# Performance work log

Measured on AMD Instinct MI355X. Metric: run time of the kernel, lower is better.

Reference implementation:

```python
import jax, jax.numpy as jnp
import numpy as np

EPS = 1e-5
NEG_SLOPE = 0.2  # GATConv default negative_slope


def layer_norm(x, g, b):
    mu = jnp.mean(x, axis=-1, keepdims=True)
    var = jnp.mean((x - mu) ** 2, axis=-1, keepdims=True)
    return (x - mu) * jax.lax.rsqrt(var + EPS) * g + b


def setup_inputs() -> dict:
    key = jax.random.key(0)
    ks = jax.random.split(key, 16)
    B, NPG = 64, 1024          # graphs, fine nodes per graph
    NF = B * NPG               # 65536 fine nodes
    IN, HID, ATT, H, LLM = 1024, 1024, 64, 8, 2048
    D = ATT * H                # 512
    w = lambda k, shp: (jax.random.normal(k, shp, jnp.float32) * 0.02)
    # structured bipartite star edges: fine node i -> global node i // NPG
    edge_index = jnp.stack([jnp.arange(NF, dtype=jnp.int32),
                            (jnp.arange(NF, dtype=jnp.int32) // NPG)])
    return {
        "x_fine": jax.random.normal(ks[0], (NF, IN), jnp.float32),
        "x_global": jax.random.normal(ks[1], (B, D), jnp.float32),
        "edge_index_fine_global": edge_index,
        "nf_g": jnp.ones((IN,), jnp.float32), "nf_b": jnp.zeros((IN,), jnp.float32),
        "ip_w1": w(ks[2], (IN, HID)), "ip_b1": jnp.zeros((HID,), jnp.float32),
        "ip_w2": w(ks[3], (HID, D)), "ip_b2": jnp.zeros((D,), jnp.float32),
        "ng_g": jnp.ones((D,), jnp.float32), "ng_b": jnp.zeros((D,), jnp.float32),
        "gat_ws": w(ks[4], (D, D)), "gat_wd": w(ks[5], (D, D)),
        "att_s": w(ks[6], (1, H, ATT)), "att_d": w(ks[7], (1, H, ATT)),
        "gat_bias": jnp.zeros((D,), jnp.float32),
        "gp_w": w(ks[8], (D, LLM)), "gp_b": jnp.zeros((LLM,), jnp.float32),
        "fp_w": w(ks[9], (D, LLM)), "fp_b": jnp.zeros((LLM,), jnp.float32),
    }


def reference(x_fine, x_global, edge_index_fine_global,
              nf_g, nf_b, ip_w1, ip_b1, ip_w2, ip_b2, ng_g, ng_b,
              gat_ws, gat_wd, att_s, att_d, gat_bias,
              gp_w, gp_b, fp_w, fp_b):
    B = x_global.shape[0]
    H = att_s.shape[1]
    C = x_global.shape[1] // H

    # fine branch: LayerNorm -> MLP projection to H*C
    xf = layer_norm(x_fine, nf_g, nf_b)
    xf = jax.nn.relu(xf @ ip_w1 + ip_b1) @ ip_w2 + ip_b2      # [NF, H*C]
    xg = layer_norm(x_global, ng_g, ng_b)                      # [B, H*C]

    # bipartite GATConv (eval mode: attention dropout disabled)
    xs = (xf @ gat_ws).reshape(-1, H, C)                       # [NF, H, C]
    xd = (xg @ gat_wd).reshape(B, H, C)                        # [B, H, C]
    a_s = jnp.sum(xs * att_s, axis=-1)                         # [NF, H]
    a_d = jnp.sum(xd * att_d, axis=-1)                         # [B, H]

    row, col = edge_index_fine_global[0], edge_index_fine_global[1]
    loops = jnp.arange(B, dtype=row.dtype)                     # add_self_loops: nodes < min(NF,B)
    rows = jnp.concatenate([row, loops])
    cols = jnp.concatenate([col, loops])
    # PyG removes pre-existing self-loop edges; emulate by masking them out
    self_mask = jnp.concatenate([row == col, jnp.zeros((B,), bool)])

    logits = jax.nn.leaky_relu(a_s[rows] + a_d[cols], NEG_SLOPE)   # [E+B, H]
    logits = jnp.where(self_mask[:, None], -jnp.inf, logits)
    m = jax.ops.segment_max(logits, cols, num_segments=B)         # [B, H]
    e = jnp.exp(logits - m[cols])
    e = jnp.where(self_mask[:, None], 0.0, e)
    denom = jax.ops.segment_sum(e, cols, num_segments=B)
    alpha = e / denom[cols]                                       # [E+B, H]

    msg = xs[rows] * alpha[..., None]                              # [E+B, H, C]
    agg = jax.ops.segment_sum(msg, cols, num_segments=B)          # [B, H, C]
    xg = agg.reshape(B, H * C) + gat_bias + xg                    # GAT out + residual

    og = (xg @ gp_w + gp_b)[:, None, :]                            # [B, 1, LLM]
    of = (xf @ fp_w + fp_b).reshape(B, -1, fp_w.shape[1])          # [B, NPG, LLM]
    return jnp.concatenate([og, of], axis=1)                       # [B, 1+NPG, LLM]
```

## Files before the change

### kernel.cpp

```cpp
#include <hip/hip_runtime.h>
#include <hip/hip_bf16.h>
#include <math.h>

typedef __bf16 bf16_t;
typedef bf16_t bf16x8 __attribute__((ext_vector_type(8)));
typedef bf16_t bf16x4 __attribute__((ext_vector_type(4)));
typedef float f32x4 __attribute__((ext_vector_type(4)));

#define DEVINL __device__ __forceinline__

DEVINL float wave_reduce_sum(float v) {
#pragma unroll
  for (int o = 32; o > 0; o >>= 1) v += __shfl_down(v, o);
  return v;
}
DEVINL float wave_reduce_max(float v) {
#pragma unroll
  for (int o = 32; o > 0; o >>= 1) v = fmaxf(v, __shfl_down(v, o));
  return v;
}
DEVINL float block_reduce_sum256(float v, float* red) {
  int tid = threadIdx.x;
  __syncthreads();
  v = wave_reduce_sum(v);
  if ((tid & 63) == 0) red[tid >> 6] = v;
  __syncthreads();
  return red[0] + red[1] + red[2] + red[3];
}
DEVINL float block_reduce_max256(float v, float* red) {
  int tid = threadIdx.x;
  __syncthreads();
  v = wave_reduce_max(v);
  if ((tid & 63) == 0) red[tid >> 6] = v;
  __syncthreads();
  return fmaxf(fmaxf(red[0], red[1]), fmaxf(red[2], red[3]));
}

template <int CPT, bool BF16OUT>
__global__ __launch_bounds__(256) void k_ln(const float* __restrict__ x,
                                            const float* __restrict__ g,
                                            const float* __restrict__ b,
                                            void* __restrict__ out) {
  constexpr int COLS = CPT * 256;
  __shared__ float red[8];
  const size_t row = blockIdx.x;
  const float* xr = x + row * COLS;
  const int c0 = threadIdx.x * CPT;
  float v[CPT];
#pragma unroll
  for (int j = 0; j < CPT; j++) v[j] = xr[c0 + j];
  float s = 0;
#pragma unroll
  for (int j = 0; j < CPT; j++) s += v[j];
  const float mu = block_reduce_sum256(s, red) * (1.0f / COLS);
  float q = 0;
#pragma unroll
  for (int j = 0; j < CPT; j++) { float d = v[j] - mu; q += d * d; }
  const float var = block_reduce_sum256(q, red) * (1.0f / COLS);
  const float rs = rsqrtf(var + 1e-5f);
  if constexpr (BF16OUT) {
    bf16x4 o;
#pragma unroll
    for (int j = 0; j < CPT; j++)
      o[j] = (bf16_t)((v[j] - mu) * rs * g[c0 + j] + b[c0 + j]);
    *(bf16x4*)((bf16_t*)out + row * COLS + c0) = o;
  } else {
#pragma unroll
    for (int j = 0; j < CPT; j++)
      ((float*)out)[row * COLS + c0 + j] = (v[j] - mu) * rs * g[c0 + j] + b[c0 + j];
  }
}

__global__ __launch_bounds__(256) void k_tcast(const float* __restrict__ src,
                                               bf16_t* __restrict__ dst, int K, int N) {
  __shared__ float t[32][33];
  const int n0 = blockIdx.x * 32, k0 = blockIdx.y * 32;
  const int tx = threadIdx.x, ty = threadIdx.y;
#pragma unroll
  for (int i = 0; i < 32; i += 8)
    t[ty + i][tx] = src[(size_t)(k0 + ty + i) * N + n0 + tx];
  __syncthreads();
#pragma unroll
  for (int i = 0; i < 32; i += 8)
    dst[(size_t)(n0 + ty + i) * K + k0 + tx] = (bf16_t)t[tx][ty + i];
}

__global__ __launch_bounds__(256) void k_fold_wd(const float* __restrict__ gat_wd,
                                                 const float* __restrict__ att_d,
                                                 float* __restrict__ wd_att) {
  const int k = blockIdx.x * 256 + threadIdx.x;
#pragma unroll
  for (int h = 0; h < 8; h++) {
    float s = 0;
    for (int c = 0; c < 64; c++)
      s += gat_wd[(size_t)k * 512 + h * 64 + c] * att_d[h * 64 + c];
    wd_att[k * 8 + h] = s;
  }
}

template <int N, int K, int EPI>
__global__ __launch_bounds__(256, 2) void gemm_bt(const bf16_t* __restrict__ A,
                                                  const bf16_t* __restrict__ Bt,
                                                  const float* __restrict__ bias,
                                                  void* __restrict__ Cout) {
  __shared__ bf16_t As[128 * 64];
  __shared__ bf16_t Bs[128 * 64];
  const int tid = threadIdx.x;
  const int lane = tid & 63;
  const int wid = tid >> 6;
  const int wm = wid >> 1, wn = wid & 1;
  const size_t arow0 = (size_t)blockIdx.x * 128;
  const int bcol0 = blockIdx.y * 128;

  f32x4 acc[4][4] = {};
  const int kTiles = K / 64;
  for (int kt = 0; kt < kTiles; ++kt) {
    const int k0 = kt * 64;
#pragma unroll
    for (int i = 0; i < 4; ++i) {
      const int c = i * 256 + tid;
      const int r = c >> 3, kc = (c & 7) * 8;
      const bf16_t* ga = A + (arow0 + r) * K + k0 + kc;
      __builtin_amdgcn_global_load_lds(
          (const __attribute__((address_space(1))) void*)ga,
          (__attribute__((address_space(3))) void*)(As + c * 8), 16, 0, 0);
      const bf16_t* gb = Bt + ((size_t)bcol0 + r) * K + k0 + kc;
      __builtin_amdgcn_global_load_lds(
          (const __attribute__((address_space(1))) void*)gb,
          (__attribute__((address_space(3))) void*)(Bs + c * 8), 16, 0, 0);
    }
    __syncthreads();
#pragma unroll
    for (int kk = 0; kk < 2; ++kk) {
      bf16x8 af[4], bfr[4];
      const int kofs = kk * 32 + (lane >> 4) * 8;
#pragma unroll
      for (int m = 0; m < 4; ++m)
        af[m] = *(const bf16x8*)(As + (wm * 64 + m * 16 + (lane & 15)) * 64 + kofs);
#pragma unroll
      for (int n = 0; n < 4; ++n)
        bfr[n] = *(const bf16x8*)(Bs + (wn * 64 + n * 16 + (lane & 15)) * 64 + kofs);
#pragma unroll
      for (int m = 0; m < 4; ++m)
#pragma unroll
        for (int n = 0; n < 4; ++n)
          acc[m][n] = __builtin_amdgcn_mfma_f32_16x16x32_bf16(af[m], bfr[n], acc[m][n], 0, 0, 0);
    }
    __syncthreads();
  }
  const int lr = (lane >> 4) * 4;
  const int lc = lane & 15;
#pragma unroll
  for (int n = 0; n < 4; ++n) {
    const int col = bcol0 + wn * 64 + n * 16 + lc;
    const float bv = (EPI == 2) ? 0.0f : bias[col];
#pragma unroll
    for (int m = 0; m < 4; ++m) {
#pragma unroll
      for (int j = 0; j < 4; ++j) {
        const size_t row = arow0 + wm * 64 + m * 16 + lr + j;
        float v = acc[m][n][j] + bv;
        if constexpr (EPI == 0) v = v > 0.0f ? v : 0.0f;
        if constexpr (EPI == 3) {
          const size_t orow = row + (row >> 10) + 1;
          ((float*)Cout)[orow * (size_t)N + col] = v;
        } else {
          ((bf16_t*)Cout)[row * (size_t)N + col] = (bf16_t)v;
        }
      }
    }
  }
}

__global__ __launch_bounds__(256) void k_attn(const bf16_t* __restrict__ xs,
                                              const float* __restrict__ xg,
                                              const float* __restrict__ wd_att,
                                              const float* __restrict__ att_s,
                                              float* __restrict__ agg) {
  const int b = blockIdx.x >> 3, h = blockIdx.x & 7;
  const int tid = threadIdx.x;
  __shared__ float sl[1024];
  __shared__ float part[256];
  __shared__ float red[8];
  __shared__ float s_att[64];
  __shared__ float s_sc[4];
  if (tid < 64) s_att[tid] = att_s[h * 64 + tid];
  float pa = 0;
#pragma unroll
  for (int kk = 0; kk < 2; kk++) {
    const int k = tid + kk * 256;
    pa += xg[b * 512 + k] * wd_att[k * 8 + h];
  }
  const float a_d = block_reduce_sum256(pa, red);
  const bf16_t* xsb = xs + ((size_t)b * 1024) * 512 + h * 64;
#pragma unroll
  for (int j = 0; j < 4; j++) {
    const int i = tid + j * 256;
    const bf16_t* xr = xsb + (size_t)i * 512;
    float s = 0;
#pragma unroll
    for (int c = 0; c < 64; c += 8) {
      bf16x8 v = *(const bf16x8*)(xr + c);
#pragma unroll
      for (int u = 0; u < 8; u++) s += (float)v[u] * s_att[c + u];
    }
    const float lg = s + a_d;
    sl[i] = lg > 0.0f ? lg : 0.2f * lg;
  }
  if (tid == 0) {
    float self_lg = -INFINITY;
    if (b != 0) {
      const bf16_t* xr = xs + (size_t)b * 512 + h * 64;
      float s = 0;
      for (int c = 0; c < 64; c++) s += (float)xr[c] * s_att[c];
      const float lg = s + a_d;
      self_lg = lg > 0.0f ? lg : 0.2f * lg;
    }
    s_sc[0] = self_lg;
  }
  __syncthreads();
  float mx = -1e30f;
#pragma unroll
  for (int j = 0; j < 4; j++) mx = fmaxf(mx, sl[tid + j * 256]);
  mx = block_reduce_max256(mx, red);
  const float m = fmaxf(mx, s_sc[0]);
  float ps = 0;
#pragma unroll
  for (int j = 0; j < 4; j++) {
    const int i = tid + j * 256;
    const float e = __expf(sl[i] - m);
    sl[i] = e;
    ps += e;
  }
  if (tid == 0) s_sc[1] = __expf(s_sc[0] - m);
  const float dsum = block_reduce_sum256(ps, red);
  const float e_self = s_sc[1];
  const float inv = 1.0f / (dsum + e_self);
  const int c = tid & 63, grp = tid >> 6;
  float acc = 0;
  const bf16_t* xcol = xs + ((size_t)b * 1024) * 512 + h * 64 + c;
  for (int i = grp * 256; i < grp * 256 + 256; i++)
    acc += sl[i] * (float)xcol[(size_t)i * 512];
  if (grp == 0) acc += e_self * (float)xs[(size_t)b * 512 + h * 64 + c];
  part[tid] = acc;
  __syncthreads();
  if (tid < 64) {
    const float t = part[tid] + part[tid + 64] + part[tid + 128] + part[tid + 192];
    agg[(size_t)b * 512 + h * 64 + tid] = t * inv;
  }
}

__global__ __launch_bounds__(256) void k_og(const float* __restrict__ agg,
                                            const float* __restrict__ gat_bias,
                                            const float* __restrict__ xg,
                                            const float* __restrict__ gp_w,
                                            const float* __restrict__ gp_b,
                                            float* __restrict__ out) {
  __shared__ float xv[512];
  const int b = blockIdx.y;
  const int c = blockIdx.x * 256 + threadIdx.x;
  for (int k = threadIdx.x; k < 512; k += 256)
    xv[k] = agg[b * 512 + k] + gat_bias[k] + xg[b * 512 + k];
  __syncthreads();
  float acc = gp_b[c];
#pragma unroll 8
  for (int k = 0; k < 512; k++) acc += xv[k] * gp_w[(size_t)k * 2048 + c];
  out[(size_t)b * 1025 * 2048 + c] = acc;
}

extern "C" void kernel_launch(void* const* d_in, const int* in_sizes, int n_in,
                              void* d_out, int out_size, void* d_ws, size_t ws_size,
                              hipStream_t stream) {
  const float* x_fine   = (const float*)d_in[0];
  const float* x_global = (const float*)d_in[1];
  const float* nf_g  = (const float*)d_in[3];
  const float* nf_b  = (const float*)d_in[4];
  const float* ip_w1 = (const float*)d_in[5];
  const float* ip_b1 = (const float*)d_in[6];
  const float* ip_w2 = (const float*)d_in[7];
  const float* ip_b2 = (const float*)d_in[8];
  const float* ng_g  = (const float*)d_in[9];
  const float* ng_b  = (const float*)d_in[10];
  const float* gat_ws   = (const float*)d_in[11];
  const float* gat_wd   = (const float*)d_in[12];
  const float* att_s    = (const float*)d_in[13];
  const float* att_d    = (const float*)d_in[14];
  const float* gat_bias = (const float*)d_in[15];
  const float* gp_w = (const float*)d_in[16];
  const float* gp_b = (const float*)d_in[17];
  const float* fp_w = (const float*)d_in[18];
  const float* fp_b = (const float*)d_in[19];
  float* out = (float*)d_out;

  char* ws = (char*)d_ws;
  bf16_t* xf_ln = (bf16_t*)ws;
  bf16_t* hbuf  = (bf16_t*)(ws + 134217728ULL);
  char* sm = ws + 268435456ULL;
  bf16_t* w1t = (bf16_t*)sm;
  bf16_t* w2t = (bf16_t*)(sm + 2097152ULL);
  bf16_t* wst = (bf16_t*)(sm + 3145728ULL);
  bf16_t* fpt = (bf16_t*)(sm + 3670016ULL);
  float*  xg  = (float*)(sm + 5767168ULL);
  float*  wd_att = (float*)(sm + 5898240ULL);
  float*  aggp   = (float*)(sm + 5914624ULL);
  bf16_t* xf  = xf_ln;
  bf16_t* xsb = hbuf;

  k_tcast<<<dim3(32, 32), dim3(32, 8), 0, stream>>>(ip_w1, w1t, 1024, 1024);
  k_tcast<<<dim3(16, 32), dim3(32, 8), 0, stream>>>(ip_w2, w2t, 1024, 512);
  k_tcast<<<dim3(16, 16), dim3(32, 8), 0, stream>>>(gat_ws, wst, 512, 512);
  k_tcast<<<dim3(64, 16), dim3(32, 8), 0, stream>>>(fp_w, fpt, 512, 2048);
  k_fold_wd<<<2, 256, 0, stream>>>(gat_wd, att_d, wd_att);

  k_ln<4, true><<<65536, 256, 0, stream>>>(x_fine, nf_g, nf_b, xf_ln);
  k_ln<2, false><<<64, 256, 0, stream>>>(x_global, ng_g, ng_b, xg);

  gemm_bt<1024, 1024, 0><<<dim3(512, 8), 256, 0, stream>>>(xf_ln, w1t, ip_b1, hbuf);
  gemm_bt<512, 1024, 1><<<dim3(512, 4), 256, 0, stream>>>(hbuf, w2t, ip_b2, xf);
  gemm_bt<512, 512, 2><<<dim3(512, 4), 256, 0, stream>>>(xf, wst, nullptr, xsb);

  k_attn<<<512, 256, 0, stream>>>(xsb, xg, wd_att, att_s, aggp);
  k_og<<<dim3(8, 64), 256, 0, stream>>>(aggp, gat_bias, xg, gp_w, gp_b, out);

  gemm_bt<2048, 512, 3><<<dim3(512, 16), 256, 0, stream>>>(xf, fpt, fp_b, out);
}
```

Measured before the change: 849.1 us.

## Fold GAT source projection into attention and use persistent double-buffered GEMM

```diff
diff --git a/kernel.cpp b/kernel.cpp
--- a/kernel.cpp
+++ b/kernel.cpp
@@ -14,11 +14,6 @@
   for (int o = 32; o > 0; o >>= 1) v += __shfl_down(v, o);
   return v;
 }
-DEVINL float wave_reduce_max(float v) {
-#pragma unroll
-  for (int o = 32; o > 0; o >>= 1) v = fmaxf(v, __shfl_down(v, o));
-  return v;
-}
 DEVINL float block_reduce_sum256(float v, float* red) {
   int tid = threadIdx.x;
   __syncthreads();
@@ -26,14 +21,6 @@
   if ((tid & 63) == 0) red[tid >> 6] = v;
   __syncthreads();
   return red[0] + red[1] + red[2] + red[3];
-}
-DEVINL float block_reduce_max256(float v, float* red) {
-  int tid = threadIdx.x;
-  __syncthreads();
-  v = wave_reduce_max(v);
-  if ((tid & 63) == 0) red[tid >> 6] = v;
-  __syncthreads();
-  return fmaxf(fmaxf(red[0], red[1]), fmaxf(red[2], red[3]));
 }
 
 template <int CPT, bool BF16OUT>
@@ -85,182 +72,254 @@
     dst[(size_t)(n0 + ty + i) * K + k0 + tx] = (bf16_t)t[tx][ty + i];
 }
 
-__global__ __launch_bounds__(256) void k_fold_wd(const float* __restrict__ gat_wd,
-                                                 const float* __restrict__ att_d,
-                                                 float* __restrict__ wd_att) {
+__global__ __launch_bounds__(256) void k_fold(const float* __restrict__ W,
+                                              const float* __restrict__ att,
+                                              float* __restrict__ out) {
   const int k = blockIdx.x * 256 + threadIdx.x;
 #pragma unroll
   for (int h = 0; h < 8; h++) {
     float s = 0;
     for (int c = 0; c < 64; c++)
-      s += gat_wd[(size_t)k * 512 + h * 64 + c] * att_d[h * 64 + c];
-    wd_att[k * 8 + h] = s;
+      s += W[(size_t)k * 512 + h * 64 + c] * att[h * 64 + c];
+    out[k * 8 + h] = s;
   }
 }
 
 template <int N, int K, int EPI>
-__global__ __launch_bounds__(256, 2) void gemm_bt(const bf16_t* __restrict__ A,
+__global__ __launch_bounds__(256, 2) void gemm_pm(const bf16_t* __restrict__ A,
                                                   const bf16_t* __restrict__ Bt,
                                                   const float* __restrict__ bias,
                                                   void* __restrict__ Cout) {
-  __shared__ bf16_t As[128 * 64];
-  __shared__ bf16_t Bs[128 * 64];
-  const int tid = threadIdx.x;
-  const int lane = tid & 63;
-  const int wid = tid >> 6;
+  constexpr int NBY = N / 128;
+  constexpr int WPC = 512 / NBY;
+  constexpr int TPW = 512 / WPC;
+  constexpr int nt = K / 64;
+  constexpr int NSTEP = TPW * nt;
+  __shared__ __align__(16) bf16_t As[2][8192];
+  __shared__ __align__(16) bf16_t Bs[2][8192];
+  const int w = blockIdx.x;
+  const int by = w % NBY;
+  const int mchunk = w / NBY;
+  const int tid = threadIdx.x, lane = tid & 63, wid = tid >> 6;
   const int wm = wid >> 1, wn = wid & 1;
-  const size_t arow0 = (size_t)blockIdx.x * 128;
-  const int bcol0 = blockIdx.y * 128;
+  const int bcol0 = by * 128;
+  const size_t mbase = (size_t)mchunk * TPW * 128;
+
+  int s_r[4], s_c[4];
+#pragma unroll
+  for (int i = 0; i < 4; i++) {
+    const int q = i * 256 + tid;
+    s_r[i] = q >> 3;
+    s_c[i] = ((q & 7) ^ ((q >> 3) & 7)) * 8;
+  }
+  const int l15 = lane & 15, l7 = lane & 7, lq = lane >> 4;
+  const int e0 = (lq ^ l7) * 8;
+  const int e1 = ((4 + lq) ^ l7) * 8;
+
+  float bv[4];
+#pragma unroll
+  for (int n = 0; n < 4; n++)
+    bv[n] = (EPI == 2) ? 0.0f : bias[bcol0 + wn * 64 + n * 16 + l15];
 
   f32x4 acc[4][4] = {};
-  const int kTiles = K / 64;
-  for (int kt = 0; kt < kTiles; ++kt) {
-    const int k0 = kt * 64;
-#pragma unroll
-    for (int i = 0; i < 4; ++i) {
-      const int c = i * 256 + tid;
-      const int r = c >> 3, kc = (c & 7) * 8;
-      const bf16_t* ga = A + (arow0 + r) * K + k0 + kc;
-      __builtin_amdgcn_global_load_lds(
-          (const __attribute__((address_space(1))) void*)ga,
-          (__attribute__((address_space(3))) void*)(As + c * 8), 16, 0, 0);
-      const bf16_t* gb = Bt + ((size_t)bcol0 + r) * K + k0 + kc;
-      __builtin_amdgcn_global_load_lds(
-          (const __attribute__((address_space(1))) void*)gb,
-          (__attribute__((address_space(3))) void*)(Bs + c * 8), 16, 0, 0);
-    }
-    __syncthreads();
-#pragma unroll
-    for (int kk = 0; kk < 2; ++kk) {
-      bf16x8 af[4], bfr[4];
-      const int kofs = kk * 32 + (lane >> 4) * 8;
-#pragma unroll
-      for (int m = 0; m < 4; ++m)
-        af[m] = *(const bf16x8*)(As + (wm * 64 + m * 16 + (lane & 15)) * 64 + kofs);
-#pragma unroll
-      for (int n = 0; n < 4; ++n)
-        bfr[n] = *(const bf16x8*)(Bs + (wn * 64 + n * 16 + (lane & 15)) * 64 + kofs);
-#pragma unroll
-      for (int m = 0; m < 4; ++m)
-#pragma unroll
-        for (int n = 0; n < 4; ++n)
-          acc[m][n] = __builtin_amdgcn_mfma_f32_16x16x32_bf16(af[m], bfr[n], acc[m][n], 0, 0, 0);
-    }
-    __syncthreads();
-  }
-  const int lr = (lane >> 4) * 4;
-  const int lc = lane & 15;
-#pragma unroll
-  for (int n = 0; n < 4; ++n) {
-    const int col = bcol0 + wn * 64 + n * 16 + lc;
-    const float bv = (EPI == 2) ? 0.0f : bias[col];
-#pragma unroll
-    for (int m = 0; m < 4; ++m) {
-#pragma unroll
-      for (int j = 0; j < 4; ++j) {
-        const size_t row = arow0 + wm * 64 + m * 16 + lr + j;
-        float v = acc[m][n][j] + bv;
-        if constexpr (EPI == 0) v = v > 0.0f ? v : 0.0f;
-        if constexpr (EPI == 3) {
-          const size_t orow = row + (row >> 10) + 1;
-          ((float*)Cout)[orow * (size_t)N + col] = v;
-        } else {
-          ((bf16_t*)Cout)[row * (size_t)N + col] = (bf16_t)v;
+
+#define STG(s, bb)                                                                   \
+  {                                                                                  \
+    const int _t = (s) / nt, _kt = (s) % nt;                                         \
+    _Pragma("unroll") for (int _i = 0; _i < 4; _i++) {                               \
+      const bf16_t* _ga =                                                            \
+          A + (mbase + _t * 128 + s_r[_i]) * (size_t)K + _kt * 64 + s_c[_i];         \
+      __builtin_amdgcn_global_load_lds(                                              \
+          (const __attribute__((address_space(1))) void*)_ga,                        \
+          (__attribute__((address_space(3))) void*)&As[bb][(_i * 256 + tid) * 8],    \
+          16, 0, 0);                                                                 \
+      const bf16_t* _gb =                                                            \
+          Bt + ((size_t)bcol0 + s_r[_i]) * (size_t)K + _kt * 64 + s_c[_i];           \
+      __builtin_amdgcn_global_load_lds(                                              \
+          (const __attribute__((address_space(1))) void*)_gb,                        \
+          (__attribute__((address_space(3))) void*)&Bs[bb][(_i * 256 + tid) * 8],    \
+          16, 0, 0);                                                                 \
+    }                                                                                \
+  }
+
+  STG(0, 0);
+  for (int s = 0; s < NSTEP; ++s) {
+    if (s + 1 < NSTEP) {
+      STG(s + 1, (s + 1) & 1);
+      asm volatile("s_waitcnt vmcnt(8)" ::: "memory");
+    } else {
+      asm volatile("s_waitcnt vmcnt(0)" ::: "memory");
+    }
+    __builtin_amdgcn_s_barrier();
+    const int b = s & 1;
+    bf16x8 af0[4], af1[4], bf0[4], bf1[4];
+#pragma unroll
+    for (int m = 0; m < 4; m++) {
+      const bf16_t* p = &As[b][(wm * 64 + m * 16 + l15) * 64];
+      af0[m] = *(const bf16x8*)(p + e0);
+      af1[m] = *(const bf16x8*)(p + e1);
+    }
+#pragma unroll
+    for (int n = 0; n < 4; n++) {
+      const bf16_t* p = &Bs[b][(wn * 64 + n * 16 + l15) * 64];
+      bf0[n] = *(const bf16x8*)(p + e0);
+      bf1[n] = *(const bf16x8*)(p + e1);
+    }
+#pragma unroll
+    for (int m = 0; m < 4; m++)
+#pragma unroll
+      for (int n = 0; n < 4; n++) {
+        acc[m][n] = __builtin_amdgcn_mfma_f32_16x16x32_bf16(af0[m], bf0[n], acc[m][n], 0, 0, 0);
+        acc[m][n] = __builtin_amdgcn_mfma_f32_16x16x32_bf16(af1[m], bf1[n], acc[m][n], 0, 0, 0);
+      }
+    if ((s & (nt - 1)) == nt - 1) {
+      const int t = s / nt;
+      const int lr = lq * 4;
+#pragma unroll
+      for (int n = 0; n < 4; n++) {
+        const int col = bcol0 + wn * 64 + n * 16 + l15;
+#pragma unroll
+        for (int m = 0; m < 4; m++) {
+#pragma unroll
+          for (int j = 0; j < 4; j++) {
+            const size_t row = mbase + (size_t)t * 128 + wm * 64 + m * 16 + lr + j;
+            float v = acc[m][n][j] + bv[n];
+            if (EPI == 0) v = v > 0.0f ? v : 0.0f;
+            if (EPI == 3) {
+              const size_t orow = row + (row >> 10) + 1;
+              ((float*)Cout)[orow * (size_t)N + col] = v;
+            } else {
+              ((bf16_t*)Cout)[row * (size_t)N + col] = (bf16_t)v;
+            }
+            acc[m][n][j] = 0.0f;
+          }
         }
       }
     }
-  }
-}
-
-__global__ __launch_bounds__(256) void k_attn(const bf16_t* __restrict__ xs,
-                                              const float* __restrict__ xg,
-                                              const float* __restrict__ wd_att,
-                                              const float* __restrict__ att_s,
-                                              float* __restrict__ agg) {
-  const int b = blockIdx.x >> 3, h = blockIdx.x & 7;
-  const int tid = threadIdx.x;
-  __shared__ float sl[1024];
-  __shared__ float part[256];
-  __shared__ float red[8];
-  __shared__ float s_att[64];
-  __shared__ float s_sc[4];
-  if (tid < 64) s_att[tid] = att_s[h * 64 + tid];
+    __builtin_amdgcn_s_barrier();
+  }
+#undef STG
+}
+
+__global__ __launch_bounds__(256) void k_as(const bf16_t* __restrict__ xf,
+                                            const float* __restrict__ wsatt,
+                                            float* __restrict__ a_s) {
+  const int tid = threadIdx.x, l = tid & 63, wid = tid >> 6;
+  float wreg[64];
+#pragma unroll
+  for (int q = 0; q < 16; q++) {
+    const float4 v = *(const float4*)(wsatt + l * 64 + q * 4);
+    wreg[q * 4 + 0] = v.x; wreg[q * 4 + 1] = v.y;
+    wreg[q * 4 + 2] = v.z; wreg[q * 4 + 3] = v.w;
+  }
+  const size_t base = (size_t)blockIdx.x * 128 + wid * 32;
+  for (int rr = 0; rr < 32; rr++) {
+    const size_t i = base + rr;
+    const bf16x8 v = *(const bf16x8*)(xf + i * 512 + l * 8);
+    float p[8] = {};
+#pragma unroll
+    for (int u = 0; u < 8; u++) {
+      const float xv = (float)v[u];
+#pragma unroll
+      for (int h = 0; h < 8; h++) p[h] += xv * wreg[u * 8 + h];
+    }
+#pragma unroll
+    for (int h = 0; h < 8; h++)
+#pragma unroll
+      for (int mk = 1; mk < 64; mk <<= 1) p[h] += __shfl_xor(p[h], mk);
+    float outv = 0.0f;
+#pragma unroll
+    for (int h = 0; h < 8; h++) outv = (l == h) ? p[h] : outv;
+    if (l < 8) a_s[i * 8 + l] = outv;
+  }
+}
+
+__global__ __launch_bounds__(512) void k_alpha_z(const float* __restrict__ a_s,
+                                                 const bf16_t* __restrict__ xf,
+                                                 const float* __restrict__ xg,
+                                                 const float* __restrict__ wd_att,
+                                                 float* __restrict__ z) {
+  __shared__ float sal[8][1028];
+  const int b = blockIdx.x;
+  const int tid = threadIdx.x, l = tid & 63, h = tid >> 6;
   float pa = 0;
 #pragma unroll
-  for (int kk = 0; kk < 2; kk++) {
-    const int k = tid + kk * 256;
-    pa += xg[b * 512 + k] * wd_att[k * 8 + h];
-  }
-  const float a_d = block_reduce_sum256(pa, red);
-  const bf16_t* xsb = xs + ((size_t)b * 1024) * 512 + h * 64;
-#pragma unroll
-  for (int j = 0; j < 4; j++) {
-    const int i = tid + j * 256;
-    const bf16_t* xr = xsb + (size_t)i * 512;
-    float s = 0;
-#pragma unroll
-    for (int c = 0; c < 64; c += 8) {
-      bf16x8 v = *(const bf16x8*)(xr + c);
-#pragma unroll
-      for (int u = 0; u < 8; u++) s += (float)v[u] * s_att[c + u];
-    }
-    const float lg = s + a_d;
-    sl[i] = lg > 0.0f ? lg : 0.2f * lg;
-  }
-  if (tid == 0) {
-    float self_lg = -INFINITY;
-    if (b != 0) {
-      const bf16_t* xr = xs + (size_t)b * 512 + h * 64;
-      float s = 0;
-      for (int c = 0; c < 64; c++) s += (float)xr[c] * s_att[c];
-      const float lg = s + a_d;
-      self_lg = lg > 0.0f ? lg : 0.2f * lg;
-    }
-    s_sc[0] = self_lg;
-  }
-  __syncthreads();
-  float mx = -1e30f;
-#pragma unroll
-  for (int j = 0; j < 4; j++) mx = fmaxf(mx, sl[tid + j * 256]);
-  mx = block_reduce_max256(mx, red);
-  const float m = fmaxf(mx, s_sc[0]);
+  for (int u = 0; u < 8; u++)
+    pa += xg[b * 512 + l * 8 + u] * wd_att[(l * 8 + u) * 8 + h];
+#pragma unroll
+  for (int mk = 1; mk < 64; mk <<= 1) pa += __shfl_xor(pa, mk);
+  const float ad = pa;
+  const float* asb = a_s + (size_t)b * 1024 * 8;
+  float lg[16];
+  float lmax = -1e30f;
+#pragma unroll
+  for (int j = 0; j < 16; j++) {
+    const float a = asb[(l + j * 64) * 8 + h] + ad;
+    lg[j] = a > 0.0f ? a : 0.2f * a;
+    lmax = fmaxf(lmax, lg[j]);
+  }
+  float lself = -INFINITY;
+  if (l == 0 && b != 0) {
+    const float a = a_s[b * 8 + h] + ad;
+    lself = a > 0.0f ? a : 0.2f * a;
+  }
+  lmax = fmaxf(lmax, lself);
+#pragma unroll
+  for (int mk = 1; mk < 64; mk <<= 1) lmax = fmaxf(lmax, __shfl_xor(lmax, mk));
   float ps = 0;
 #pragma unroll
-  for (int j = 0; j < 4; j++) {
-    const int i = tid + j * 256;
-    const float e = __expf(sl[i] - m);
-    sl[i] = e;
-    ps += e;
-  }
-  if (tid == 0) s_sc[1] = __expf(s_sc[0] - m);
-  const float dsum = block_reduce_sum256(ps, red);
-  const float e_self = s_sc[1];
-  const float inv = 1.0f / (dsum + e_self);
-  const int c = tid & 63, grp = tid >> 6;
+  for (int j = 0; j < 16; j++) { lg[j] = __expf(lg[j] - lmax); ps += lg[j]; }
+  const float eself = (l == 0 && lself != -INFINITY) ? __expf(lself - lmax) : 0.0f;
+  ps += eself;
+#pragma unroll
+  for (int mk = 1; mk < 64; mk <<= 1) ps += __shfl_xor(ps, mk);
+  const float inv = 1.0f / ps;
+#pragma unroll
+  for (int j = 0; j < 16; j++) sal[h][l + j * 64] = lg[j] * inv;
+  if (l == 0) sal[h][1024] = eself * inv;
+  __syncthreads();
+  float zp[8] = {};
+  const bf16_t* xb = xf + (size_t)b * 1024 * 512 + l * 8;
+  for (int i = 0; i < 1024; i++) {
+    const float a = sal[h][i];
+    const bf16x8 v = *(const bf16x8*)(xb + (size_t)i * 512);
+#pragma unroll
+    for (int u = 0; u < 8; u++) zp[u] += a * (float)v[u];
+  }
+  {
+    const float a = sal[h][1024];
+    const bf16x8 v = *(const bf16x8*)(xf + (size_t)b * 512 + l * 8);
+#pragma unroll
+    for (int u = 0; u < 8; u++) zp[u] += a * (float)v[u];
+  }
+  float4 o0 = {zp[0], zp[1], zp[2], zp[3]};
+  float4 o1 = {zp[4], zp[5], zp[6], zp[7]};
+  float* zo = z + ((size_t)b * 8 + h) * 512 + l * 8;
+  *(float4*)zo = o0;
+  *(float4*)(zo + 4) = o1;
+}
+
+__global__ __launch_bounds__(512) void k_fin(const float* __restrict__ z,
+                                             const float* __restrict__ ws,
+                                             const float* __restrict__ gat_bias,
+                                             const float* __restrict__ xg,
+                                             float* __restrict__ aggx) {
+  const int b = blockIdx.x, c = threadIdx.x, h = c >> 6;
+  const float* zr = z + ((size_t)b * 8 + h) * 512;
   float acc = 0;
-  const bf16_t* xcol = xs + ((size_t)b * 1024) * 512 + h * 64 + c;
-  for (int i = grp * 256; i < grp * 256 + 256; i++)
-    acc += sl[i] * (float)xcol[(size_t)i * 512];
-  if (grp == 0) acc += e_self * (float)xs[(size_t)b * 512 + h * 64 + c];
-  part[tid] = acc;
-  __syncthreads();
-  if (tid < 64) {
-    const float t = part[tid] + part[tid + 64] + part[tid + 128] + part[tid + 192];
-    agg[(size_t)b * 512 + h * 64 + tid] = t * inv;
-  }
-}
-
-__global__ __launch_bounds__(256) void k_og(const float* __restrict__ agg,
-                                            const float* __restrict__ gat_bias,
-                                            const float* __restrict__ xg,
+#pragma unroll 8
+  for (int k = 0; k < 512; k++) acc += zr[k] * ws[(size_t)k * 512 + c];
+  aggx[b * 512 + c] = acc + gat_bias[c] + xg[b * 512 + c];
+}
+
+__global__ __launch_bounds__(256) void k_og(const float* __restrict__ aggx,
                                             const float* __restrict__ gp_w,
                                             const float* __restrict__ gp_b,
                                             float* __restrict__ out) {
   __shared__ float xv[512];
   const int b = blockIdx.y;
   const int c = blockIdx.x * 256 + threadIdx.x;
-  for (int k = threadIdx.x; k < 512; k += 256)
-    xv[k] = agg[b * 512 + k] + gat_bias[k] + xg[b * 512 + k];
+  for (int k = threadIdx.x; k < 512; k += 256) xv[k] = aggx[b * 512 + k];
   __syncthreads();
   float acc = gp_b[c];
 #pragma unroll 8
@@ -296,31 +355,33 @@
   bf16_t* xf_ln = (bf16_t*)ws;
   bf16_t* hbuf  = (bf16_t*)(ws + 134217728ULL);
   char* sm = ws + 268435456ULL;
-  bf16_t* w1t = (bf16_t*)sm;
-  bf16_t* w2t = (bf16_t*)(sm + 2097152ULL);
-  bf16_t* wst = (bf16_t*)(sm + 3145728ULL);
-  bf16_t* fpt = (bf16_t*)(sm + 3670016ULL);
-  float*  xg  = (float*)(sm + 5767168ULL);
-  float*  wd_att = (float*)(sm + 5898240ULL);
-  float*  aggp   = (float*)(sm + 5914624ULL);
-  bf16_t* xf  = xf_ln;
-  bf16_t* xsb = hbuf;
+  bf16_t* w1t  = (bf16_t*)sm;
+  bf16_t* w2t  = (bf16_t*)(sm + 2097152ULL);
+  bf16_t* fpt  = (bf16_t*)(sm + 3145728ULL);
+  float*  a_s  = (float*)(sm + 5242880ULL);
+  float*  xg   = (float*)(sm + 7340032ULL);
+  float*  wd_att = (float*)(sm + 7471104ULL);
+  float*  wsatt  = (float*)(sm + 7487488ULL);
+  float*  zbuf   = (float*)(sm + 7503872ULL);
+  float*  aggx   = (float*)(sm + 8552448ULL);
+  bf16_t* xf = xf_ln;
 
   k_tcast<<<dim3(32, 32), dim3(32, 8), 0, stream>>>(ip_w1, w1t, 1024, 1024);
   k_tcast<<<dim3(16, 32), dim3(32, 8), 0, stream>>>(ip_w2, w2t, 1024, 512);
-  k_tcast<<<dim3(16, 16), dim3(32, 8), 0, stream>>>(gat_ws, wst, 512, 512);
   k_tcast<<<dim3(64, 16), dim3(32, 8), 0, stream>>>(fp_w, fpt, 512, 2048);
-  k_fold_wd<<<2, 256, 0, stream>>>(gat_wd, att_d, wd_att);
+  k_fold<<<2, 256, 0, stream>>>(gat_wd, att_d, wd_att);
+  k_fold<<<2, 256, 0, stream>>>(gat_ws, att_s, wsatt);
 
   k_ln<4, true><<<65536, 256, 0, stream>>>(x_fine, nf_g, nf_b, xf_ln);
   k_ln<2, false><<<64, 256, 0, stream>>>(x_global, ng_g, ng_b, xg);
 
-  gemm_bt<1024, 1024, 0><<<dim3(512, 8), 256, 0, stream>>>(xf_ln, w1t, ip_b1, hbuf);
-  gemm_bt<512, 1024, 1><<<dim3(512, 4), 256, 0, stream>>>(hbuf, w2t, ip_b2, xf);
-  gemm_bt<512, 512, 2><<<dim3(512, 4), 256, 0, stream>>>(xf, wst, nullptr, xsb);
-
-  k_attn<<<512, 256, 0, stream>>>(xsb, xg, wd_att, att_s, aggp);
-  k_og<<<dim3(8, 64), 256, 0, stream>>>(aggp, gat_bias, xg, gp_w, gp_b, out);
-
-  gemm_bt<2048, 512, 3><<<dim3(512, 16), 256, 0, stream>>>(xf, fpt, fp_b, out);
-}
+  gemm_pm<1024, 1024, 0><<<512, 256, 0, stream>>>(xf_ln, w1t, ip_b1, hbuf);
+  gemm_pm<512, 1024, 1><<<512, 256, 0, stream>>>(hbuf, w2t, ip_b2, xf);
+
+  k_as<<<512, 256, 0, stream>>>(xf, wsatt, a_s);
+  k_alpha_z<<<64, 512, 0, stream>>>(a_s, xf, xg, wd_att, zbuf);
+  k_fin<<<64, 512, 0, stream>>>(zbuf, gat_ws, gat_bias, xg, aggx);
+  k_og<<<dim3(8, 64), 256, 0, stream>>>(aggx, gp_w, gp_b, out);
+
+  gemm_pm<2048, 512, 3><<<512, 256, 0, stream>>>(xf, fpt, fp_b, out);
+}
```

New measurement: 953.8 us. +12.3%, slower.
